# Kernel optimization log

Hardware: AMD Instinct MI355X
Metric: run time of the kernel (lower is better)

The kernel has to match this reference:

```python
import jax, jax.numpy as jnp
from jax import lax
import numpy as np

INPUT, HIDDEN, OUTPUT, SEQ = 1024, 1024, 1024, 8192


def setup_inputs() -> dict:
    key = jax.random.key(0)
    ks = jax.random.split(key, 7)
    s = 1.0 / np.sqrt(HIDDEN)
    return {
        "input_seq": jax.random.normal(ks[0], (SEQ, INPUT), dtype=jnp.float32),
        # PyTorch nn.LSTM params, gate order [i, f, g, o]
        "W_ih": jax.random.uniform(ks[1], (4 * HIDDEN, INPUT), jnp.float32, -s, s),
        "W_hh": jax.random.uniform(ks[2], (4 * HIDDEN, HIDDEN), jnp.float32, -s, s),
        "b_ih": jax.random.uniform(ks[3], (4 * HIDDEN,), jnp.float32, -s, s),
        "b_hh": jax.random.uniform(ks[4], (4 * HIDDEN,), jnp.float32, -s, s),
        "W_out": jax.random.uniform(ks[5], (OUTPUT, HIDDEN), jnp.float32, -s, s),
        "b_out": jax.random.uniform(ks[6], (OUTPUT,), jnp.float32, -s, s),
    }


def reference(input_seq, W_ih, W_hh, b_ih, b_hh, W_out, b_out):
    H = W_hh.shape[1]
    # Precompute input projections for all timesteps in one GEMM: [S, 4H]
    x_gates = input_seq @ W_ih.T + (b_ih + b_hh)

    def step(carry, xg):
        h, c = carry
        gates = xg + h @ W_hh.T                      # [4H]
        i = jax.nn.sigmoid(gates[:H])
        f = jax.nn.sigmoid(gates[H:2 * H])
        g = jnp.tanh(gates[2 * H:3 * H])
        o = jax.nn.sigmoid(gates[3 * H:])
        c = f * c + i * g
        h = o * jnp.tanh(c)
        return (h, c), None

    h0 = jnp.zeros((H,), dtype=input_seq.dtype)
    (h_final, _), _ = lax.scan(step, (h0, h0), x_gates)
    # Original applies linear per-timestep then takes predictions[-1];
    # linear is pointwise in time, so projecting only h_final is identical math.
    return h_final @ W_out.T + b_out
```

## Files before the change

kernel.cpp:

```cpp
#include <hip/hip_runtime.h>
#include <hip/hip_fp16.h>

typedef _Float16 h2v __attribute__((ext_vector_type(2)));

__device__ __forceinline__ float fdot2(unsigned int a, unsigned int b, float c) {
    return __builtin_amdgcn_fdot2(__builtin_bit_cast(h2v, a),
                                  __builtin_bit_cast(h2v, b), c, false);
}

#define SCOPE_SYS __HIP_MEMORY_SCOPE_SYSTEM

__global__ __launch_bounds__(256) void k_f2h(const float* __restrict__ src,
                                             __half* __restrict__ dst, int n4) {
    int i = blockIdx.x * 256 + threadIdx.x;
    if (i >= n4) return;
    float4 v = ((const float4*)src)[i];
    union { __half2 h[2]; uint2 u; } o;
    o.h[0] = __halves2half2(__float2half_rn(v.x), __float2half_rn(v.y));
    o.h[1] = __halves2half2(__float2half_rn(v.z), __float2half_rn(v.w));
    ((uint2*)dst)[i] = o.u;
}

__global__ __launch_bounds__(256) void k_bias(const float* __restrict__ a,
                                              const float* __restrict__ b,
                                              float* __restrict__ o) {
    int i = blockIdx.x * 256 + threadIdx.x;
    if (i < 4096) o[i] = a[i] + b[i];
}

__global__ __launch_bounds__(256) void k_gemm_xg(const __half* __restrict__ A,
                                                 const __half* __restrict__ B,
                                                 const float* __restrict__ bias,
                                                 __half* __restrict__ C) {
    __shared__ unsigned int As[128][20];
    __shared__ unsigned int Bs[128][20];
    const int tid = threadIdx.x;
    const int tx = tid & 15, ty = tid >> 4;
    const int m0 = blockIdx.x * 128, n0 = blockIdx.y * 128;
    float acc[8][8];
#pragma unroll
    for (int i = 0; i < 8; ++i)
#pragma unroll
        for (int j = 0; j < 8; ++j) acc[i][j] = 0.f;
    const unsigned int* Ag = (const unsigned int*)(A + (size_t)m0 * 1024);
    const unsigned int* Bg = (const unsigned int*)(B + (size_t)n0 * 1024);
    for (int k0 = 0; k0 < 512; k0 += 16) {
        __syncthreads();
#pragma unroll
        for (int j = 0; j < 2; ++j) {
            int qd = j * 256 + tid;
            int row = qd >> 2;
            int c4 = (qd & 3) << 2;
            uint4 va = *(const uint4*)(Ag + (size_t)row * 512 + k0 + c4);
            uint4 vb = *(const uint4*)(Bg + (size_t)row * 512 + k0 + c4);
            *(uint4*)&As[row][c4] = va;
            *(uint4*)&Bs[row][c4] = vb;
        }
        __syncthreads();
#pragma unroll
        for (int k2 = 0; k2 < 16; k2 += 2) {
            unsigned int a0[8], a1[8], b0[8], b1[8];
#pragma unroll
            for (int i = 0; i < 8; ++i) {
                uint2 v = *(const uint2*)&As[ty + 16 * i][k2];
                a0[i] = v.x; a1[i] = v.y;
            }
#pragma unroll
            for (int j = 0; j < 8; ++j) {
                uint2 v = *(const uint2*)&Bs[tx + 16 * j][k2];
                b0[j] = v.x; b1[j] = v.y;
            }
#pragma unroll
            for (int i = 0; i < 8; ++i)
#pragma unroll
                for (int j = 0; j < 8; ++j) {
                    acc[i][j] = fdot2(a0[i], b0[j], acc[i][j]);
                    acc[i][j] = fdot2(a1[i], b1[j], acc[i][j]);
                }
        }
    }
#pragma unroll
    for (int i = 0; i < 8; ++i) {
        int row = m0 + ty + 16 * i;
#pragma unroll
        for (int j = 0; j < 8; ++j) {
            int col = n0 + tx + 16 * j;
            C[(size_t)row * 4096 + col] = __float2half_rn(acc[i][j] + bias[col]);
        }
    }
}

__global__ __launch_bounds__(512, 1) void k_lstm(const __half* __restrict__ Whh,
                                                 const __half* __restrict__ xg,
                                                 unsigned int* pub) {
    __shared__ unsigned int hs[2][544];
    const int tid = threadIdx.x;
    const int b = blockIdx.x;
    const int w = tid >> 6, lane = tid & 63;
    const int rho = lane >> 2;
    const int cc = lane & 3;
    const int grow = (rho & 3) * 1024 + b * 32 + 4 * w + (rho >> 2);
    uint4 wr[32];
#pragma unroll
    for (int i = 0; i < 32; ++i)
        wr[i] = *(const uint4*)(Whh + (size_t)grow * 1024 + cc * 256 + i * 8);
    const int soff = (tid >> 6) * 68 + (tid & 63);
    const int upub = b * 32 + w * 4 + (lane >> 4);
    float c_state = 0.f;
    __syncthreads();

    for (int t = 0; t < 8192; ++t) {
        float xv = __half2float(xg[(size_t)t * 4096 + grow]);
        unsigned int d = 0;
        if (t > 0) {
            const unsigned long long* src =
                (const unsigned long long*)(pub + (((t - 1) & 1) << 10)) + tid;
            const unsigned tt = (unsigned)t;
            unsigned long long v = __hip_atomic_load(src, __ATOMIC_RELAXED, SCOPE_SYS);
            unsigned lo = (unsigned)v, hi = (unsigned)(v >> 32);
            while ((lo >> 16) != tt || (hi >> 16) != tt) {
                v = __hip_atomic_load(src, __ATOMIC_RELAXED, SCOPE_SYS);
                lo = (unsigned)v; hi = (unsigned)(v >> 32);
            }
            d = (lo & 0xffffu) | (hi << 16);
        }
        const int p = t & 1;
        hs[p][soff] = d;
        __syncthreads();
        float acc = 0.f;
        const unsigned int* hsp = &hs[p][cc * 136];
#pragma unroll
        for (int i = 0; i < 32; ++i) {
            uint4 h4 = *(const uint4*)(hsp + (i >> 4) * 68 + ((i & 15) << 2));
            acc = fdot2(wr[i].x, h4.x, acc);
            acc = fdot2(wr[i].y, h4.y, acc);
            acc = fdot2(wr[i].z, h4.z, acc);
            acc = fdot2(wr[i].w, h4.w, acc);
        }
        acc += __shfl_xor(acc, 1);
        acc += __shfl_xor(acc, 2);
        acc += xv;
        const int base = lane & 48;
        float gi = __shfl(acc, base + 0);
        float gf = __shfl(acc, base + 4);
        float gg = __shfl(acc, base + 8);
        float go = __shfl(acc, base + 12);
        gi = 1.f / (1.f + __expf(-gi));
        gf = 1.f / (1.f + __expf(-gf));
        gg = 2.f / (1.f + __expf(-2.f * gg)) - 1.f;
        go = 1.f / (1.f + __expf(-go));
        c_state = gf * c_state + gi * gg;
        float hval = go * (2.f / (1.f + __expf(-2.f * c_state)) - 1.f);
        if ((lane & 15) == 0) {
            unsigned val = ((unsigned)(t + 1) << 16) |
                           (unsigned)__half_as_ushort(__float2half_rn(hval));
            __hip_atomic_store(pub + (p << 10) + upub, val,
                               __ATOMIC_RELAXED, SCOPE_SYS);
        }
    }
}

__global__ __launch_bounds__(256) void k_proj(const unsigned int* __restrict__ hfin,
                                              const float* __restrict__ Wout,
                                              const float* __restrict__ bout,
                                              float* __restrict__ out) {
    __shared__ float red[256];
    const int o = blockIdx.x, tid = threadIdx.x;
    const float* wr = Wout + (size_t)o * 1024;
    float acc = 0.f;
#pragma unroll
    for (int j = 0; j < 4; ++j) {
        int e = j * 256 + tid;
        unsigned v = hfin[e];
        acc += __half2float(__ushort_as_half((unsigned short)(v & 0xffffu))) * wr[e];
    }
    red[tid] = acc;
    __syncthreads();
    for (int s = 128; s > 0; s >>= 1) {
        if (tid < s) red[tid] += red[tid + s];
        __syncthreads();
    }
    if (tid == 0) out[o] = red[0] + bout[o];
}

extern "C" void kernel_launch(void* const* d_in, const int* in_sizes, int n_in,
                              void* d_out, int out_size, void* d_ws, size_t ws_size,
                              hipStream_t stream) {
    const float* input_seq = (const float*)d_in[0];
    const float* W_ih = (const float*)d_in[1];
    const float* W_hh = (const float*)d_in[2];
    const float* b_ih = (const float*)d_in[3];
    const float* b_hh = (const float*)d_in[4];
    const float* W_out = (const float*)d_in[5];
    const float* b_out = (const float*)d_in[6];
    float* out = (float*)d_out;

    char* ws = (char*)d_ws;
    unsigned int* pub = (unsigned int*)ws;
    float* bias = (float*)(ws + 24576);
    __half* Wih_h = (__half*)(ws + 65536);
    __half* Whh_h = (__half*)(ws + 65536 + (size_t)8 * 1024 * 1024);
    __half* in_h  = (__half*)(ws + 65536 + (size_t)16 * 1024 * 1024);
    __half* xg    = (__half*)(ws + 65536 + (size_t)32 * 1024 * 1024);

    hipMemsetAsync(ws, 0, 8192, stream);

    k_f2h<<<8192, 256, 0, stream>>>(input_seq, in_h, 2 * 1024 * 1024);
    k_f2h<<<4096, 256, 0, stream>>>(W_ih, Wih_h, 1024 * 1024);
    k_f2h<<<4096, 256, 0, stream>>>(W_hh, Whh_h, 1024 * 1024);
    k_bias<<<16, 256, 0, stream>>>(b_ih, b_hh, bias);

    dim3 gg(64, 32);
    k_gemm_xg<<<gg, 256, 0, stream>>>(in_h, Wih_h, bias, xg);

    k_lstm<<<32, 512, 0, stream>>>(Whh_h, xg, pub);

    k_proj<<<1024, 256, 0, stream>>>(pub + 1024, W_out, b_out, out);
}
```

Measured before the change: 20.70 ms.

## Spread LSTM recurrence over 64 blocks with W_hh slice held in LDS

The persistent LSTM kernel now runs on 64 workgroups instead of 32, each owning 16 hidden units. Each thread keeps its W_hh slice in shared memory (128 KB per block) instead of in 32 uint4 registers, and the dot product uses 8 lanes per gate row with four independent accumulators. The goal is to halve the per-step matvec work on each block and cut the serial dependency chain in the recurrence. In exchange, more blocks must join the cross-block spin barrier every step, and the weights are reread from LDS each step.

Result: slower. 24.02 ms (+16.0%).

```diff
diff --git a/kernel.cpp b/kernel.cpp
--- a/kernel.cpp
+++ b/kernel.cpp
@@ -93,19 +93,20 @@
 __global__ __launch_bounds__(512, 1) void k_lstm(const __half* __restrict__ Whh,
                                                  const __half* __restrict__ xg,
                                                  unsigned int* pub) {
+    __shared__ uint4 Wp[16][512];
     __shared__ unsigned int hs[2][544];
     const int tid = threadIdx.x;
     const int b = blockIdx.x;
     const int w = tid >> 6, lane = tid & 63;
-    const int rho = lane >> 2;
-    const int cc = lane & 3;
-    const int grow = (rho & 3) * 1024 + b * 32 + 4 * w + (rho >> 2);
-    uint4 wr[32];
-#pragma unroll
-    for (int i = 0; i < 32; ++i)
-        wr[i] = *(const uint4*)(Whh + (size_t)grow * 1024 + cc * 256 + i * 8);
+    const int rho = lane >> 3;
+    const int cc = lane & 7;
+    const int grow = (rho & 3) * 1024 + b * 16 + 2 * w + (rho >> 2);
+    const unsigned int* gw = (const unsigned int*)(Whh + (size_t)grow * 1024 + cc * 128);
+#pragma unroll
+    for (int i = 0; i < 16; ++i)
+        Wp[i][tid] = *(const uint4*)(gw + i * 4);
     const int soff = (tid >> 6) * 68 + (tid & 63);
-    const int upub = b * 32 + w * 4 + (lane >> 4);
+    const int upub = b * 16 + w * 2 + (lane >> 5);
     float c_state = 0.f;
     __syncthreads();
 
@@ -127,31 +128,44 @@
         const int p = t & 1;
         hs[p][soff] = d;
         __syncthreads();
-        float acc = 0.f;
-        const unsigned int* hsp = &hs[p][cc * 136];
-#pragma unroll
-        for (int i = 0; i < 32; ++i) {
-            uint4 h4 = *(const uint4*)(hsp + (i >> 4) * 68 + ((i & 15) << 2));
-            acc = fdot2(wr[i].x, h4.x, acc);
-            acc = fdot2(wr[i].y, h4.y, acc);
-            acc = fdot2(wr[i].z, h4.z, acc);
-            acc = fdot2(wr[i].w, h4.w, acc);
-        }
+        float a0 = 0.f, a1 = 0.f, a2 = 0.f, a3 = 0.f;
+        const unsigned int* hsp = &hs[p][cc * 68];
+#pragma unroll
+        for (int i = 0; i < 16; i += 4) {
+            uint4 w0 = Wp[i + 0][tid];
+            uint4 w1 = Wp[i + 1][tid];
+            uint4 w2 = Wp[i + 2][tid];
+            uint4 w3 = Wp[i + 3][tid];
+            uint4 h0 = *(const uint4*)(hsp + (i + 0) * 4);
+            uint4 h1 = *(const uint4*)(hsp + (i + 1) * 4);
+            uint4 h2 = *(const uint4*)(hsp + (i + 2) * 4);
+            uint4 h3 = *(const uint4*)(hsp + (i + 3) * 4);
+            a0 = fdot2(w0.x, h0.x, a0); a1 = fdot2(w0.y, h0.y, a1);
+            a2 = fdot2(w0.z, h0.z, a2); a3 = fdot2(w0.w, h0.w, a3);
+            a0 = fdot2(w1.x, h1.x, a0); a1 = fdot2(w1.y, h1.y, a1);
+            a2 = fdot2(w1.z, h1.z, a2); a3 = fdot2(w1.w, h1.w, a3);
+            a0 = fdot2(w2.x, h2.x, a0); a1 = fdot2(w2.y, h2.y, a1);
+            a2 = fdot2(w2.z, h2.z, a2); a3 = fdot2(w2.w, h2.w, a3);
+            a0 = fdot2(w3.x, h3.x, a0); a1 = fdot2(w3.y, h3.y, a1);
+            a2 = fdot2(w3.z, h3.z, a2); a3 = fdot2(w3.w, h3.w, a3);
+        }
+        float acc = (a0 + a1) + (a2 + a3);
         acc += __shfl_xor(acc, 1);
         acc += __shfl_xor(acc, 2);
+        acc += __shfl_xor(acc, 4);
         acc += xv;
-        const int base = lane & 48;
+        const int base = lane & 32;
         float gi = __shfl(acc, base + 0);
-        float gf = __shfl(acc, base + 4);
-        float gg = __shfl(acc, base + 8);
-        float go = __shfl(acc, base + 12);
+        float gf = __shfl(acc, base + 8);
+        float gg = __shfl(acc, base + 16);
+        float go = __shfl(acc, base + 24);
         gi = 1.f / (1.f + __expf(-gi));
         gf = 1.f / (1.f + __expf(-gf));
         gg = 2.f / (1.f + __expf(-2.f * gg)) - 1.f;
         go = 1.f / (1.f + __expf(-go));
         c_state = gf * c_state + gi * gg;
         float hval = go * (2.f / (1.f + __expf(-2.f * c_state)) - 1.f);
-        if ((lane & 15) == 0) {
+        if ((lane & 31) == 0) {
             unsigned val = ((unsigned)(t + 1) << 16) |
                            (unsigned)__half_as_ushort(__float2half_rn(hval));
             __hip_atomic_store(pub + (p << 10) + upub, val,
@@ -213,7 +227,7 @@
     dim3 gg(64, 32);
     k_gemm_xg<<<gg, 256, 0, stream>>>(in_h, Wih_h, bias, xg);
 
-    k_lstm<<<32, 512, 0, stream>>>(Whh_h, xg, pub);
+    k_lstm<<<64, 512, 0, stream>>>(Whh_h, xg, pub);
 
     k_proj<<<1024, 256, 0, stream>>>(pub + 1024, W_out, b_out, out);
 }
```
